# Optimization experiments

Measured on AMD Instinct MI355X. Metric: run time of the kernel, lower is better.

The kernel has to match this reference:

```python
import jax, jax.numpy as jnp
import numpy as np

B, S, D = 2, 2048, 1024
H = 16
HD = D // H


def setup_inputs() -> dict:
    key = jax.random.key(0)
    ks = jax.random.split(key, 6)
    X = jax.random.normal(ks[0], (B, S, D), dtype=jnp.float32)
    # Linear weights stored [in, out] so y = x @ W (torch stores transposed).
    sc = 1.0 / np.sqrt(D)
    Wq = jax.random.normal(ks[1], (D, D), dtype=jnp.float32) * sc
    Wk = jax.random.normal(ks[2], (D, D), dtype=jnp.float32) * sc
    Wv = jax.random.normal(ks[3], (D, D), dtype=jnp.float32) * sc
    Wo = jax.random.normal(ks[4], (D, D), dtype=jnp.float32) * sc
    bo = jax.random.normal(ks[5], (D,), dtype=jnp.float32) * 0.01
    return {"X": X, "Wq": Wq, "Wk": Wk, "Wv": Wv, "Wo": Wo, "bo": bo}


def reference(X, Wq, Wk, Wv, Wo, bo):
    b, n, _ = X.shape
    # QKV projections (no bias, qkv_bias=False), reshape to [b, h, n, hd]
    q = (X @ Wq).reshape(b, n, H, HD).transpose(0, 2, 1, 3)
    k = (X @ Wk).reshape(b, n, H, HD).transpose(0, 2, 1, 3)
    v = (X @ Wv).reshape(b, n, H, HD).transpose(0, 2, 1, 3)
    # Unscaled scores (module's scale flag defaults to False)
    scores = jnp.einsum("bhqd,bhkd->bhqk", q, k)
    causal = jnp.triu(jnp.ones((n, n), dtype=bool), k=1)  # True above diagonal
    scores = jnp.where(causal, -jnp.inf, scores)
    attn = jax.nn.softmax(scores, axis=-1)
    # dropout p=0.0 -> identity
    ctx = jnp.einsum("bhqk,bhkd->bqhd", attn, v).reshape(b, n, H * HD)
    return ctx @ Wo + bo
```

## Files before the change

### kernel.cpp

```cpp
#include <hip/hip_runtime.h>
#include <stdint.h>


typedef __attribute__((ext_vector_type(8))) short short8;
typedef __attribute__((ext_vector_type(4))) float floatx4;

#define S_LEN 2048
#define D_DIM 1024
#define NH 16
#define HD 64
#define L2E 1.44269504088896340736f

__device__ __forceinline__ short f2bf(float f) {
    uint32_t u = __builtin_bit_cast(uint32_t, f);
    uint32_t r = u + 0x7fffu + ((u >> 16) & 1u);
    return (short)(r >> 16);
}
__device__ __forceinline__ uint32_t pack2(float a, float b) {
    return (uint32_t)(uint16_t)f2bf(a) | ((uint32_t)(uint16_t)f2bf(b) << 16);
}
__device__ __forceinline__ void gll16(const void* g, void* l) {
    __builtin_amdgcn_global_load_lds(
        (const __attribute__((address_space(1))) void*)g,
        (__attribute__((address_space(3))) void*)l, 16, 0, 0);
}

__global__ __launch_bounds__(256) void castx_kernel(const float* __restrict__ X,
                                                    short* __restrict__ Xb) {
    int i = blockIdx.x * 256 + threadIdx.x;
    const float4 v = *(const float4*)(X + (size_t)i * 4);
    short4 o;
    o.x = f2bf(v.x); o.y = f2bf(v.y); o.z = f2bf(v.z); o.w = f2bf(v.w);
    *(short4*)(Xb + (size_t)i * 4) = o;
}

__global__ __launch_bounds__(256) void tcast_kernel(const float* __restrict__ W,
                                                    short* __restrict__ WT) {
    __shared__ float tile[32][33];
    const int bx = blockIdx.x * 32;
    const int by = blockIdx.y * 32;
    const int tx = threadIdx.x, ty = threadIdx.y;
    for (int i = 0; i < 32; i += 8)
        tile[ty + i][tx] = W[(size_t)(bx + ty + i) * D_DIM + by + tx];
    __syncthreads();
    for (int i = 0; i < 32; i += 8)
        WT[(size_t)(by + ty + i) * D_DIM + bx + tx] = f2bf(tile[tx][ty + i]);
}

__device__ __forceinline__ void gemm_main(const short* __restrict__ A,
                                          const short* __restrict__ BT,
                                          short* As, short* Bs,
                                          int m0, int n0, floatx4 (&acc)[4][4],
                                          int tid) {
    const int lane = tid & 63, ln = lane & 15, quad = lane >> 4;
    const int wave = tid >> 6;
    const int mw = (wave & 1) * 64, nw = (wave >> 1) * 64;
    for (int k0 = 0; k0 < D_DIM; k0 += 64) {
        __syncthreads();
        for (int t = 0; t < 4; t++) {
            const int c = t * 256 + tid;
            const int row = c >> 3, pos = c & 7, src = pos ^ (row & 7);
            gll16(A  + (size_t)(m0 + row) * D_DIM + k0 + src * 8, As + c * 8);
            gll16(BT + (size_t)(n0 + row) * D_DIM + k0 + src * 8, Bs + c * 8);
        }
        __syncthreads();
        for (int ks = 0; ks < 2; ks++) {
            short8 a[4], b[4];
            const int pos = ((ks * 4) ^ 0);
            for (int i = 0; i < 4; i++) {
                const int row = mw + i * 16 + ln;
                a[i] = *(const short8*)(As + row * 64 + (((ks * 4 + quad) ^ (ln & 7)) * 8));
                (void)pos;
            }
            for (int j = 0; j < 4; j++) {
                const int row = nw + j * 16 + ln;
                b[j] = *(const short8*)(Bs + row * 64 + (((ks * 4 + quad) ^ (ln & 7)) * 8));
            }
            for (int i = 0; i < 4; i++)
                for (int j = 0; j < 4; j++)
                    acc[i][j] = __builtin_amdgcn_mfma_f32_16x16x32_bf16(a[i], b[j], acc[i][j], 0, 0, 0);
        }
    }
}

__global__ __launch_bounds__(256) void gemm_qkv_kernel(const short* __restrict__ Xb,
                                                       const short* __restrict__ WT,
                                                       short* __restrict__ Qb,
                                                       short* __restrict__ Kb,
                                                       short* __restrict__ Vtb) {
    __shared__ __align__(16) short As[128 * 64];
    __shared__ __align__(16) short Bs[128 * 64];
    const int m0 = blockIdx.x * 128, n0 = blockIdx.y * 128;
    floatx4 acc[4][4] = {};
    gemm_main(Xb, WT, As, Bs, m0, n0, acc, threadIdx.x);

    const int tid = threadIdx.x, wave = tid >> 6, lane = tid & 63;
    const int ln = lane & 15, quad = lane >> 4;
    const int mw = (wave & 1) * 64, nw = (wave >> 1) * 64;
    const int nsel = n0 >> 10;
    short* outB = (nsel == 0) ? Qb : (nsel == 1 ? Kb : Vtb);
    for (int i = 0; i < 4; i++)
        for (int j = 0; j < 4; j++)
            for (int r = 0; r < 4; r++) {
                const int row = m0 + mw + i * 16 + quad * 4 + r;
                const int col = (n0 & 1023) + nw + j * 16 + ln;
                const int bb = row >> 11, s = row & (S_LEN - 1);
                const int h = col >> 6, hd = col & (HD - 1);
                const short v = f2bf(acc[i][j][r]);
                if (nsel < 2)
                    outB[(((size_t)(bb * NH + h)) * S_LEN + s) * HD + hd] = v;
                else
                    outB[(((size_t)(bb * NH + h)) * HD + hd) * S_LEN + s] = v;
            }
}

__global__ __launch_bounds__(256) void gemm_out_kernel(const short* __restrict__ Cb,
                                                       const short* __restrict__ WoT,
                                                       float* __restrict__ out,
                                                       const float* __restrict__ bias) {
    __shared__ __align__(16) short As[128 * 64];
    __shared__ __align__(16) short Bs[128 * 64];
    const int m0 = blockIdx.x * 128, n0 = blockIdx.y * 128;
    floatx4 acc[4][4] = {};
    gemm_main(Cb, WoT, As, Bs, m0, n0, acc, threadIdx.x);

    const int tid = threadIdx.x, wave = tid >> 6, lane = tid & 63;
    const int ln = lane & 15, quad = lane >> 4;
    const int mw = (wave & 1) * 64, nw = (wave >> 1) * 64;
    for (int i = 0; i < 4; i++)
        for (int j = 0; j < 4; j++)
            for (int r = 0; r < 4; r++) {
                const int row = m0 + mw + i * 16 + quad * 4 + r;
                const int col = n0 + nw + j * 16 + ln;
                out[(size_t)row * D_DIM + col] = acc[i][j][r] + bias[col];
            }
}

__global__ __launch_bounds__(256) void attn_kernel(const short* __restrict__ Q,
                                                   const short* __restrict__ Kg,
                                                   const short* __restrict__ Vt,
                                                   short* __restrict__ ctx) {
    __shared__ __align__(16) short Ks[64 * 64];
    __shared__ __align__(16) short Vs[64 * 64];
    __shared__ __align__(16) short Ps[4][16 * 72];

    const int tid = threadIdx.x, wave = tid >> 6, lane = tid & 63;
    const int ln = lane & 15, quad = lane >> 4;
    const int bh = blockIdx.y, bb = bh >> 4, h = bh & 15;

    for (int half = 0; half < 2; half++) {
        const int qt = half ? (31 - blockIdx.x) : blockIdx.x;
        const int q0 = qt * 64;

        const short* qrow = Q + ((size_t)bh * S_LEN + q0 + wave * 16 + ln) * HD;
        const short8 qb0 = *(const short8*)(qrow + quad * 8);
        const short8 qb1 = *(const short8*)(qrow + 32 + quad * 8);

        float m_run = -INFINITY, l_run = 0.f;
        floatx4 o_acc[4] = {};

        for (int kt = 0; kt <= qt; kt++) {
            const int k0 = kt * 64;
            __syncthreads();
            for (int t = 0; t < 2; t++) {
                const int c = t * 256 + tid;
                const int row = c >> 3, pos = c & 7, src = pos ^ (row & 7);
                gll16(Kg + ((size_t)bh * S_LEN + k0 + row) * HD + src * 8, Ks + c * 8);
                gll16(Vt + ((size_t)bh * HD + row) * S_LEN + k0 + src * 8, Vs + c * 8);
            }
            __syncthreads();

            floatx4 sc[4];
            for (int nt = 0; nt < 4; nt++) {
                const int row = nt * 16 + ln;
                const short8 ak0 = *(const short8*)(Ks + row * 64 + ((quad ^ (ln & 7)) * 8));
                const short8 ak1 = *(const short8*)(Ks + row * 64 + (((quad + 4) ^ (ln & 7)) * 8));
                floatx4 z = {};
                z = __builtin_amdgcn_mfma_f32_16x16x32_bf16(ak0, qb0, z, 0, 0, 0);
                z = __builtin_amdgcn_mfma_f32_16x16x32_bf16(ak1, qb1, z, 0, 0, 0);
                sc[nt] = z;
            }

            if (kt == qt) {
                const int q_abs = q0 + wave * 16 + ln;
                for (int nt = 0; nt < 4; nt++)
                    for (int r = 0; r < 4; r++)
                        if (k0 + nt * 16 + quad * 4 + r > q_abs) sc[nt][r] = -1e30f;
            }

            float mt = sc[0][0];
            for (int nt = 0; nt < 4; nt++)
                for (int r = 0; r < 4; r++) mt = fmaxf(mt, sc[nt][r]);
            mt = fmaxf(mt, __shfl_xor(mt, 16, 64));
            mt = fmaxf(mt, __shfl_xor(mt, 32, 64));
            const float mnew = fmaxf(m_run, mt);
            const float alpha = exp2f((m_run - mnew) * L2E);
            float pv[4][4], ls = 0.f;
            for (int nt = 0; nt < 4; nt++)
                for (int r = 0; r < 4; r++) {
                    const float e = exp2f((sc[nt][r] - mnew) * L2E);
                    pv[nt][r] = e; ls += e;
                }
            ls += __shfl_xor(ls, 16, 64);
            ls += __shfl_xor(ls, 32, 64);
            l_run = l_run * alpha + ls;
            m_run = mnew;
            for (int dt = 0; dt < 4; dt++)
                for (int r = 0; r < 4; r++) o_acc[dt][r] *= alpha;

            for (int nt = 0; nt < 4; nt++) {
                uint2 u;
                u.x = pack2(pv[nt][0], pv[nt][1]);
                u.y = pack2(pv[nt][2], pv[nt][3]);
                *(uint2*)&Ps[wave][ln * 72 + nt * 16 + quad * 4] = u;
            }
            const short8 bp0 = *(const short8*)&Ps[wave][ln * 72 + quad * 8];
            const short8 bp1 = *(const short8*)&Ps[wave][ln * 72 + 32 + quad * 8];

            for (int dt = 0; dt < 4; dt++) {
                const int row = dt * 16 + ln;
                const short8 av0 = *(const short8*)(Vs + row * 64 + ((quad ^ (ln & 7)) * 8));
                const short8 av1 = *(const short8*)(Vs + row * 64 + (((quad + 4) ^ (ln & 7)) * 8));
                o_acc[dt] = __builtin_amdgcn_mfma_f32_16x16x32_bf16(av0, bp0, o_acc[dt], 0, 0, 0);
                o_acc[dt] = __builtin_amdgcn_mfma_f32_16x16x32_bf16(av1, bp1, o_acc[dt], 0, 0, 0);
            }
        }

        const float rl = 1.f / l_run;
        for (int dt = 0; dt < 4; dt++) {
            uint2 u;
            u.x = pack2(o_acc[dt][0] * rl, o_acc[dt][1] * rl);
            u.y = pack2(o_acc[dt][2] * rl, o_acc[dt][3] * rl);
            *(uint2*)&Ps[wave][ln * 72 + dt * 16 + quad * 4] = u;
        }
        const int qr = lane >> 2, sg = lane & 3;
        for (int c = 0; c < 2; c++) {
            const short8 v = *(const short8*)&Ps[wave][qr * 72 + sg * 8 + c * 32];
            const int q = q0 + wave * 16 + qr;
            *(short8*)(ctx + ((size_t)bb * S_LEN + q) * D_DIM + h * HD + sg * 8 + c * 32) = v;
        }
    }
}

extern "C" void kernel_launch(void* const* d_in, const int* in_sizes, int n_in,
                              void* d_out, int out_size, void* d_ws, size_t ws_size,
                              hipStream_t stream) {
    const float* X  = (const float*)d_in[0];
    const float* Wq = (const float*)d_in[1];
    const float* Wk = (const float*)d_in[2];
    const float* Wv = (const float*)d_in[3];
    const float* Wo = (const float*)d_in[4];
    const float* bo = (const float*)d_in[5];
    float* out = (float*)d_out;

    char* ws = (char*)d_ws;
    const size_t MB = 1024 * 1024;
    short* Xb     = (short*)(ws);
    short* WqkvT  = (short*)(ws + 8  * MB);
    short* WoT    = (short*)(ws + 14 * MB);
    short* Qb     = (short*)(ws + 16 * MB);
    short* Kb     = (short*)(ws + 24 * MB);
    short* Vtb    = (short*)(ws + 32 * MB);
    short* ctxb   = (short*)(ws + 40 * MB);

    castx_kernel<<<4096, 256, 0, stream>>>(X, Xb);
    dim3 tg(32, 32), tb(32, 8);
    tcast_kernel<<<tg, tb, 0, stream>>>(Wq, WqkvT);
    tcast_kernel<<<tg, tb, 0, stream>>>(Wk, WqkvT + 1024 * 1024);
    tcast_kernel<<<tg, tb, 0, stream>>>(Wv, WqkvT + 2 * 1024 * 1024);
    tcast_kernel<<<tg, tb, 0, stream>>>(Wo, WoT);

    dim3 gq(32, 24);
    gemm_qkv_kernel<<<gq, 256, 0, stream>>>(Xb, WqkvT, Qb, Kb, Vtb);

    dim3 ga(16, 32);
    attn_kernel<<<ga, 256, 0, stream>>>(Qb, Kb, Vtb, ctxb);

    dim3 go(32, 8);
    gemm_out_kernel<<<go, 256, 0, stream>>>(ctxb, WoT, out, bo);
}
```

Baseline: 208.1 us.

## Split long causal attention tiles across blocks and merge with combine kernel

```diff
diff --git a/kernel.cpp b/kernel.cpp
--- a/kernel.cpp
+++ b/kernel.cpp
@@ -17,7 +17,12 @@
     return (short)(r >> 16);
 }
 __device__ __forceinline__ uint32_t pack2(float a, float b) {
+#if __has_builtin(__builtin_amdgcn_cvt_pk_bf16_f32)
+    auto v = __builtin_amdgcn_cvt_pk_bf16_f32(a, b);
+    uint32_t r; __builtin_memcpy(&r, &v, sizeof(r)); return r;
+#else
     return (uint32_t)(uint16_t)f2bf(a) | ((uint32_t)(uint16_t)f2bf(b) << 16);
+#endif
 }
 __device__ __forceinline__ void gll16(const void* g, void* l) {
     __builtin_amdgcn_global_load_lds(
@@ -29,13 +34,21 @@
                                                     short* __restrict__ Xb) {
     int i = blockIdx.x * 256 + threadIdx.x;
     const float4 v = *(const float4*)(X + (size_t)i * 4);
-    short4 o;
-    o.x = f2bf(v.x); o.y = f2bf(v.y); o.z = f2bf(v.z); o.w = f2bf(v.w);
-    *(short4*)(Xb + (size_t)i * 4) = o;
-}
-
-__global__ __launch_bounds__(256) void tcast_kernel(const float* __restrict__ W,
-                                                    short* __restrict__ WT) {
+    uint2 o;
+    o.x = pack2(v.x, v.y);
+    o.y = pack2(v.z, v.w);
+    *(uint2*)(Xb + (size_t)i * 4) = o;
+}
+
+__global__ __launch_bounds__(256) void tcast4_kernel(const float* __restrict__ Wq,
+                                                     const float* __restrict__ Wk,
+                                                     const float* __restrict__ Wv,
+                                                     const float* __restrict__ Wo,
+                                                     short* __restrict__ WqkvT,
+                                                     short* __restrict__ WoT) {
+    const int z = blockIdx.z;
+    const float* W = (z == 0) ? Wq : (z == 1) ? Wk : (z == 2) ? Wv : Wo;
+    short* WT = (z < 3) ? (WqkvT + (size_t)z * 1024 * 1024) : WoT;
     __shared__ float tile[32][33];
     const int bx = blockIdx.x * 32;
     const int by = blockIdx.y * 32;
@@ -66,11 +79,9 @@
         __syncthreads();
         for (int ks = 0; ks < 2; ks++) {
             short8 a[4], b[4];
-            const int pos = ((ks * 4) ^ 0);
             for (int i = 0; i < 4; i++) {
                 const int row = mw + i * 16 + ln;
                 a[i] = *(const short8*)(As + row * 64 + (((ks * 4 + quad) ^ (ln & 7)) * 8));
-                (void)pos;
             }
             for (int j = 0; j < 4; j++) {
                 const int row = nw + j * 16 + ln;
@@ -139,93 +150,120 @@
 __global__ __launch_bounds__(256) void attn_kernel(const short* __restrict__ Q,
                                                    const short* __restrict__ Kg,
                                                    const short* __restrict__ Vt,
-                                                   short* __restrict__ ctx) {
+                                                   short* __restrict__ ctx,
+                                                   float* __restrict__ Opart,
+                                                   float* __restrict__ Mlpart) {
     __shared__ __align__(16) short Ks[64 * 64];
     __shared__ __align__(16) short Vs[64 * 64];
     __shared__ __align__(16) short Ps[4][16 * 72];
 
     const int tid = threadIdx.x, wave = tid >> 6, lane = tid & 63;
     const int ln = lane & 15, quad = lane >> 4;
-    const int bh = blockIdx.y, bb = bh >> 4, h = bh & 15;
-
-    for (int half = 0; half < 2; half++) {
-        const int qt = half ? (31 - blockIdx.x) : blockIdx.x;
-        const int q0 = qt * 64;
-
-        const short* qrow = Q + ((size_t)bh * S_LEN + q0 + wave * 16 + ln) * HD;
-        const short8 qb0 = *(const short8*)(qrow + quad * 8);
-        const short8 qb1 = *(const short8*)(qrow + 32 + quad * 8);
-
-        float m_run = -INFINITY, l_run = 0.f;
-        floatx4 o_acc[4] = {};
-
-        for (int kt = 0; kt <= qt; kt++) {
-            const int k0 = kt * 64;
-            __syncthreads();
-            for (int t = 0; t < 2; t++) {
-                const int c = t * 256 + tid;
-                const int row = c >> 3, pos = c & 7, src = pos ^ (row & 7);
-                gll16(Kg + ((size_t)bh * S_LEN + k0 + row) * HD + src * 8, Ks + c * 8);
-                gll16(Vt + ((size_t)bh * HD + row) * S_LEN + k0 + src * 8, Vs + c * 8);
-            }
-            __syncthreads();
-
-            floatx4 sc[4];
-            for (int nt = 0; nt < 4; nt++) {
-                const int row = nt * 16 + ln;
-                const short8 ak0 = *(const short8*)(Ks + row * 64 + ((quad ^ (ln & 7)) * 8));
-                const short8 ak1 = *(const short8*)(Ks + row * 64 + (((quad + 4) ^ (ln & 7)) * 8));
-                floatx4 z = {};
-                z = __builtin_amdgcn_mfma_f32_16x16x32_bf16(ak0, qb0, z, 0, 0, 0);
-                z = __builtin_amdgcn_mfma_f32_16x16x32_bf16(ak1, qb1, z, 0, 0, 0);
-                sc[nt] = z;
-            }
-
-            if (kt == qt) {
-                const int q_abs = q0 + wave * 16 + ln;
-                for (int nt = 0; nt < 4; nt++)
-                    for (int r = 0; r < 4; r++)
-                        if (k0 + nt * 16 + quad * 4 + r > q_abs) sc[nt][r] = -1e30f;
-            }
-
-            float mt = sc[0][0];
+
+    const int id = blockIdx.x;
+    const int xcd = id & 7;
+    const int j = id >> 3;
+    const int bh = xcd + 8 * (j & 3);
+    const int t = j >> 2;
+    int qt, k_begin, k_end, pidx;
+    if (t < 32) {
+        qt = 31 - (t >> 1);
+        const int half = t & 1;
+        const int n = qt + 1, h0 = n >> 1;
+        k_begin = half ? h0 : 0;
+        k_end   = half ? n  : h0;
+        pidx = ((qt - 16) * 32 + bh) * 2 + half;
+    } else {
+        qt = 47 - t;
+        k_begin = 0; k_end = qt + 1;
+        pidx = -1;
+    }
+    const int q0 = qt * 64;
+    const int bb = bh >> 4, h = bh & 15;
+
+    const short* qrow = Q + ((size_t)bh * S_LEN + q0 + wave * 16 + ln) * HD;
+    const short8 qb0 = *(const short8*)(qrow + quad * 8);
+    const short8 qb1 = *(const short8*)(qrow + 32 + quad * 8);
+
+    float m_run = -INFINITY, l_run = 0.f;
+    floatx4 o_acc[4] = {};
+
+    for (int kt = k_begin; kt < k_end; kt++) {
+        const int k0 = kt * 64;
+        __syncthreads();
+        for (int tt = 0; tt < 2; tt++) {
+            const int c = tt * 256 + tid;
+            const int row = c >> 3, pos = c & 7, src = pos ^ (row & 7);
+            gll16(Kg + ((size_t)bh * S_LEN + k0 + row) * HD + src * 8, Ks + c * 8);
+            gll16(Vt + ((size_t)bh * HD + row) * S_LEN + k0 + src * 8, Vs + c * 8);
+        }
+        __syncthreads();
+
+        floatx4 sc[4];
+        for (int nt = 0; nt < 4; nt++) {
+            const int row = nt * 16 + ln;
+            const short8 ak0 = *(const short8*)(Ks + row * 64 + ((quad ^ (ln & 7)) * 8));
+            const short8 ak1 = *(const short8*)(Ks + row * 64 + (((quad + 4) ^ (ln & 7)) * 8));
+            floatx4 z = {};
+            z = __builtin_amdgcn_mfma_f32_16x16x32_bf16(ak0, qb0, z, 0, 0, 0);
+            z = __builtin_amdgcn_mfma_f32_16x16x32_bf16(ak1, qb1, z, 0, 0, 0);
+            sc[nt] = z;
+        }
+
+        if (kt == qt) {
+            const int q_abs = q0 + wave * 16 + ln;
             for (int nt = 0; nt < 4; nt++)
-                for (int r = 0; r < 4; r++) mt = fmaxf(mt, sc[nt][r]);
-            mt = fmaxf(mt, __shfl_xor(mt, 16, 64));
-            mt = fmaxf(mt, __shfl_xor(mt, 32, 64));
-            const float mnew = fmaxf(m_run, mt);
-            const float alpha = exp2f((m_run - mnew) * L2E);
-            float pv[4][4], ls = 0.f;
-            for (int nt = 0; nt < 4; nt++)
-                for (int r = 0; r < 4; r++) {
-                    const float e = exp2f((sc[nt][r] - mnew) * L2E);
-                    pv[nt][r] = e; ls += e;
-                }
-            ls += __shfl_xor(ls, 16, 64);
-            ls += __shfl_xor(ls, 32, 64);
-            l_run = l_run * alpha + ls;
-            m_run = mnew;
-            for (int dt = 0; dt < 4; dt++)
-                for (int r = 0; r < 4; r++) o_acc[dt][r] *= alpha;
-
-            for (int nt = 0; nt < 4; nt++) {
-                uint2 u;
-                u.x = pack2(pv[nt][0], pv[nt][1]);
-                u.y = pack2(pv[nt][2], pv[nt][3]);
-                *(uint2*)&Ps[wave][ln * 72 + nt * 16 + quad * 4] = u;
-            }
-            const short8 bp0 = *(const short8*)&Ps[wave][ln * 72 + quad * 8];
-            const short8 bp1 = *(const short8*)&Ps[wave][ln * 72 + 32 + quad * 8];
-
-            for (int dt = 0; dt < 4; dt++) {
-                const int row = dt * 16 + ln;
-                const short8 av0 = *(const short8*)(Vs + row * 64 + ((quad ^ (ln & 7)) * 8));
-                const short8 av1 = *(const short8*)(Vs + row * 64 + (((quad + 4) ^ (ln & 7)) * 8));
-                o_acc[dt] = __builtin_amdgcn_mfma_f32_16x16x32_bf16(av0, bp0, o_acc[dt], 0, 0, 0);
-                o_acc[dt] = __builtin_amdgcn_mfma_f32_16x16x32_bf16(av1, bp1, o_acc[dt], 0, 0, 0);
-            }
-        }
-
+                for (int r = 0; r < 4; r++)
+                    if (k0 + nt * 16 + quad * 4 + r > q_abs) sc[nt][r] = -1e30f;
+        }
+
+        float mt = sc[0][0];
+        for (int nt = 0; nt < 4; nt++)
+            for (int r = 0; r < 4; r++) mt = fmaxf(mt, sc[nt][r]);
+        mt = fmaxf(mt, __shfl_xor(mt, 16, 64));
+        mt = fmaxf(mt, __shfl_xor(mt, 32, 64));
+        const float mnew = fmaxf(m_run, mt);
+        const float alpha = exp2f((m_run - mnew) * L2E);
+        float pv[4][4], ls = 0.f;
+        for (int nt = 0; nt < 4; nt++)
+            for (int r = 0; r < 4; r++) {
+                const float e = exp2f((sc[nt][r] - mnew) * L2E);
+                pv[nt][r] = e; ls += e;
+            }
+        ls += __shfl_xor(ls, 16, 64);
+        ls += __shfl_xor(ls, 32, 64);
+        l_run = l_run * alpha + ls;
+        m_run = mnew;
+        for (int dt = 0; dt < 4; dt++)
+            for (int r = 0; r < 4; r++) o_acc[dt][r] *= alpha;
+
+        for (int nt = 0; nt < 4; nt++) {
+            uint2 u;
+            u.x = pack2(pv[nt][0], pv[nt][1]);
+            u.y = pack2(pv[nt][2], pv[nt][3]);
+            *(uint2*)&Ps[wave][ln * 72 + nt * 16 + quad * 4] = u;
+        }
+        const short8 bp0 = *(const short8*)&Ps[wave][ln * 72 + quad * 8];
+        const short8 bp1 = *(const short8*)&Ps[wave][ln * 72 + 32 + quad * 8];
+
+        for (int dt = 0; dt < 4; dt++) {
+            const int row = dt * 16 + ln;
+            const short8 av0 = *(const short8*)(Vs + row * 64 + ((quad ^ (ln & 7)) * 8));
+            const short8 av1 = *(const short8*)(Vs + row * 64 + (((quad + 4) ^ (ln & 7)) * 8));
+            o_acc[dt] = __builtin_amdgcn_mfma_f32_16x16x32_bf16(av0, bp0, o_acc[dt], 0, 0, 0);
+            o_acc[dt] = __builtin_amdgcn_mfma_f32_16x16x32_bf16(av1, bp1, o_acc[dt], 0, 0, 0);
+        }
+    }
+
+    if (pidx >= 0) {
+        float* Ob = Opart + (size_t)pidx * 4096 + (wave * 16 + ln) * 64;
+        for (int dt = 0; dt < 4; dt++)
+            *(float4*)(Ob + dt * 16 + quad * 4) = *(float4*)&o_acc[dt];
+        if (quad == 0) {
+            Mlpart[(size_t)pidx * 128 + wave * 16 + ln]      = m_run;
+            Mlpart[(size_t)pidx * 128 + 64 + wave * 16 + ln] = l_run;
+        }
+    } else {
         const float rl = 1.f / l_run;
         for (int dt = 0; dt < 4; dt++) {
             uint2 u;
@@ -236,9 +274,37 @@
         const int qr = lane >> 2, sg = lane & 3;
         for (int c = 0; c < 2; c++) {
             const short8 v = *(const short8*)&Ps[wave][qr * 72 + sg * 8 + c * 32];
-            const int q = q0 + wave * 16 + qr;
-            *(short8*)(ctx + ((size_t)bb * S_LEN + q) * D_DIM + h * HD + sg * 8 + c * 32) = v;
-        }
+            const int s = q0 + wave * 16 + qr;
+            *(short8*)(ctx + ((size_t)bb * S_LEN + s) * D_DIM + h * HD + sg * 8 + c * 32) = v;
+        }
+    }
+}
+
+__global__ __launch_bounds__(256) void combine_kernel(const float* __restrict__ Opart,
+                                                      const float* __restrict__ Mlpart,
+                                                      short* __restrict__ ctx) {
+    const int tile = blockIdx.x;
+    const int qt = 16 + (tile >> 5), bh = tile & 31;
+    const int bb = bh >> 4, h = bh & 15;
+    const int p0 = ((qt - 16) * 32 + bh) * 2;
+    const float* O0 = Opart + (size_t)p0 * 4096;
+    const float* O1 = O0 + 4096;
+    const float* ml0 = Mlpart + (size_t)p0 * 128;
+    const float* ml1 = ml0 + 128;
+    for (int e = threadIdx.x; e < 1024; e += 256) {
+        const int q = e >> 4, dseg = e & 15;
+        const float m0 = ml0[q], l0 = ml0[64 + q];
+        const float m1 = ml1[q], l1 = ml1[64 + q];
+        const float m = fmaxf(m0, m1);
+        const float a0 = exp2f((m0 - m) * L2E), a1 = exp2f((m1 - m) * L2E);
+        const float rl = 1.f / (l0 * a0 + l1 * a1);
+        const float4 x0 = *(const float4*)(O0 + q * 64 + dseg * 4);
+        const float4 x1 = *(const float4*)(O1 + q * 64 + dseg * 4);
+        uint2 u;
+        u.x = pack2((x0.x * a0 + x1.x * a1) * rl, (x0.y * a0 + x1.y * a1) * rl);
+        u.y = pack2((x0.z * a0 + x1.z * a1) * rl, (x0.w * a0 + x1.w * a1) * rl);
+        const int s = qt * 64 + q;
+        *(uint2*)(ctx + ((size_t)bb * S_LEN + s) * D_DIM + h * HD + dseg * 4) = u;
     }
 }
 
@@ -257,24 +323,23 @@
     const size_t MB = 1024 * 1024;
     short* Xb     = (short*)(ws);
     short* WqkvT  = (short*)(ws + 8  * MB);
-    short* WoT    = (short*)(ws + 14 * MB);
     short* Qb     = (short*)(ws + 16 * MB);
     short* Kb     = (short*)(ws + 24 * MB);
     short* Vtb    = (short*)(ws + 32 * MB);
     short* ctxb   = (short*)(ws + 40 * MB);
+    short* WoT    = (short*)(ws + 48 * MB);
+    float* Opart  = (float*)(ws);
+    float* Mlpart = (float*)(ws + 50 * MB);
 
     castx_kernel<<<4096, 256, 0, stream>>>(X, Xb);
-    dim3 tg(32, 32), tb(32, 8);
-    tcast_kernel<<<tg, tb, 0, stream>>>(Wq, WqkvT);
-    tcast_kernel<<<tg, tb, 0, stream>>>(Wk, WqkvT + 1024 * 1024);
-    tcast_kernel<<<tg, tb, 0, stream>>>(Wv, WqkvT + 2 * 1024 * 1024);
-    tcast_kernel<<<tg, tb, 0, stream>>>(Wo, WoT);
+    dim3 tg(32, 32, 4), tb(32, 8);
+    tcast4_kernel<<<tg, tb, 0, stream>>>(Wq, Wk, Wv, Wo, WqkvT, WoT);
 
     dim3 gq(32, 24);
     gemm_qkv_kernel<<<gq, 256, 0, stream>>>(Xb, WqkvT, Qb, Kb, Vtb);
 
-    dim3 ga(16, 32);
-    attn_kernel<<<ga, 256, 0, stream>>>(Qb, Kb, Vtb, ctxb);
+    attn_kernel<<<1536, 256, 0, stream>>>(Qb, Kb, Vtb, ctxb, Opart, Mlpart);
+    combine_kernel<<<512, 256, 0, stream>>>(Opart, Mlpart, ctxb);
 
     dim3 go(32, 8);
     gemm_out_kernel<<<go, 256, 0, stream>>>(ctxb, WoT, out, bo);
```

Measured after the change: 199.8 us. -4.0%, faster.
